# Kernel tuning notes

Measured on AMD Instinct MI355X. Metric: run time of the kernel, lower is better.

## Reference

```python
import jax, jax.numpy as jnp
import numpy as np

B, NB, C, FEAT = 2, 512, 80, 1024
FIRST_N = 128
NMS_FC = 128
POS_EMB = 64
GROUPS = 16
ATT_D = (1024, 1024, 128)
NUM_THRESH = 3
BBOX_W = (10.0, 10.0, 5.0, 5.0)
SCALE_CLAMP = float(np.log(1000.0 / 16.0))


def setup_inputs() -> dict:
    key = jax.random.key(0)
    ks = jax.random.split(key, 24)
    roi_feat = jax.random.normal(ks[0], (B * NB, FEAT), jnp.float32)
    scores = jax.random.normal(ks[1], (B * NB, C + 1), jnp.float32)
    proposal_deltas = jax.random.normal(ks[2], (B * NB, C * 4), jnp.float32) * 0.5
    xy = jax.random.uniform(ks[3], (B * NB, 2), jnp.float32) * 800.0
    wh = jax.random.uniform(ks[4], (B * NB, 2), jnp.float32) * 100.0 + 1.0
    proposal_boxes = jnp.concatenate([xy, xy + wh], axis=1)

    def lin(k, fin, fout, std=0.01):
        return jax.random.normal(k, (fin, fout), jnp.float32) * std

    return {
        'roi_feat': roi_feat,
        'scores': scores,
        'proposal_deltas': proposal_deltas,
        'proposal_boxes': proposal_boxes,
        'roi_w': lin(ks[5], FEAT, NMS_FC), 'roi_b': jnp.zeros((NMS_FC,), jnp.float32),
        'rank_w': lin(ks[6], FEAT, NMS_FC), 'rank_b': jnp.zeros((NMS_FC,), jnp.float32),
        'logit_w': lin(ks[7], NMS_FC, NUM_THRESH), 'logit_b': jnp.full((NUM_THRESH,), -3.0, jnp.float32),
        'pos_w': lin(ks[8], POS_EMB, GROUPS), 'pos_b': jnp.zeros((GROUPS,), jnp.float32),
        'q_w': lin(ks[9], NMS_FC, ATT_D[0]), 'q_b': jnp.zeros((ATT_D[0],), jnp.float32),
        'k_w': lin(ks[10], NMS_FC, ATT_D[1]), 'k_b': jnp.zeros((ATT_D[1],), jnp.float32),
        'out_w': jax.random.normal(ks[11], (GROUPS, NMS_FC, ATT_D[2] // GROUPS), jnp.float32) * 0.01,
        'out_b': jnp.zeros((ATT_D[2],), jnp.float32),
        'num_boxes': NB,
    }


def _rank_embedding():
    # sinusoidal rank embedding, dim FEAT
    fr = jnp.arange(FEAT // 2, dtype=jnp.float32)
    dim_mat = jnp.power(1000.0, (2.0 / FEAT) * fr)
    div = jnp.arange(FIRST_N, dtype=jnp.float32)[:, None] / dim_mat[None, :]
    return jnp.concatenate([jnp.sin(div), jnp.cos(div)], axis=1)  # (FIRST_N, FEAT)


def _pos_embed(boxes):
    # boxes: (FIRST_N, C, 4) -> (C, N, N, POS_EMB)
    b = jnp.transpose(boxes, (1, 0, 2))  # (C, N, 4)
    x1, y1, x2, y2 = b[..., 0], b[..., 1], b[..., 2], b[..., 3]
    w = x2 - x1 + 1.0
    h = y2 - y1 + 1.0
    cx = 0.5 * (x1 + x2)
    cy = 0.5 * (y1 + y2)
    dx = jnp.log(jnp.maximum(jnp.abs((cx[:, :, None] - cx[:, None, :]) / w[:, :, None]), 1e-3))
    dy = jnp.log(jnp.maximum(jnp.abs((cy[:, :, None] - cy[:, None, :]) / h[:, :, None]), 1e-3))
    dw = jnp.log(w[:, :, None] / w[:, None, :])
    dh = jnp.log(h[:, :, None] / h[:, None, :])
    pm = jnp.stack([dx, dy, dw, dh], axis=-1)  # (C, N, N, 4)
    fr = jnp.arange(POS_EMB // 8, dtype=jnp.float32)
    dim_mat = jnp.power(1000.0, (8.0 / POS_EMB) * fr)
    dv = (pm * 100.0)[..., None] / dim_mat  # (C, N, N, 4, POS_EMB//8)
    e = jnp.concatenate([jnp.sin(dv), jnp.cos(dv)], axis=-1)  # (C, N, N, 4, POS_EMB//4)
    return e.reshape(pm.shape[:3] + (POS_EMB,))


def reference(roi_feat, scores, proposal_deltas, proposal_boxes,
              roi_w, roi_b, rank_w, rank_b, logit_w, logit_b,
              pos_w, pos_b, q_w, q_b, k_w, k_b, out_w, out_b, num_boxes):
    deltas = jax.lax.stop_gradient(proposal_deltas)  # detached in original
    pboxes = jax.lax.stop_gradient(proposal_boxes)
    batch = deltas.shape[0] // num_boxes

    # ---- Box2BoxTransform.apply_deltas ----
    widths = pboxes[:, 2] - pboxes[:, 0]
    heights = pboxes[:, 3] - pboxes[:, 1]
    ctr_x = pboxes[:, 0] + 0.5 * widths
    ctr_y = pboxes[:, 1] + 0.5 * heights
    wx, wy, ww, wh = BBOX_W
    d = deltas.reshape(-1, C, 4)
    dx = d[..., 0] / wx
    dy = d[..., 1] / wy
    dw = jnp.minimum(d[..., 2] / ww, SCALE_CLAMP)
    dh = jnp.minimum(d[..., 3] / wh, SCALE_CLAMP)
    pcx = dx * widths[:, None] + ctr_x[:, None]
    pcy = dy * heights[:, None] + ctr_y[:, None]
    pw = jnp.exp(dw) * widths[:, None]
    ph = jnp.exp(dh) * heights[:, None]
    refined = jnp.stack([pcx - 0.5 * pw, pcy - 0.5 * ph, pcx + 0.5 * pw, pcy + 0.5 * ph], axis=-1)
    refined = refined.reshape(batch, num_boxes, C, 4)

    # ---- softmax + per-class descending sort, keep first_n ----
    sc = scores.reshape(batch, num_boxes, C + 1)
    probs = jax.nn.softmax(sc[..., :C], axis=1)
    rank_idxs = jnp.argsort(-probs, axis=1)[:, :FIRST_N, :]  # (B, FIRST_N, C)
    sorted_score = jnp.take_along_axis(probs, rank_idxs, axis=1)  # (B, FIRST_N, C)
    sorted_boxes = jax.vmap(lambda bx, i: jnp.take_along_axis(bx, i[..., None], axis=0))(refined, rank_idxs)  # (B, FIRST_N, C, 4)

    # ---- rank + roi embeddings ----
    rank_feat = _rank_embedding() @ rank_w + rank_b  # (FIRST_N, NMS_FC)
    roi_emb = (roi_feat @ roi_w + roi_b).reshape(batch, num_boxes, NMS_FC)
    sorted_roi = jax.vmap(lambda e, i: e[i])(roi_emb, rank_idxs)  # (B, FIRST_N, C, NMS_FC)
    emb_feat = sorted_roi + rank_feat[None, :, None, :]

    dq = ATT_D[0] // GROUPS
    dk = ATT_D[1] // GROUPS

    def attend(feat, boxes):
        # feat: (FIRST_N, C, NMS_FC), boxes: (FIRST_N, C, 4)
        pe = _pos_embed(boxes)  # (C, N, N, POS_EMB)
        aff_w = jax.nn.relu(pe @ pos_w + pos_b)  # (C, N, N, G)
        aff_w = jnp.transpose(aff_w, (0, 3, 1, 2))  # (C, G, N, N)
        f = jnp.transpose(feat, (1, 0, 2))  # (C, N, NMS_FC)
        q = (f @ q_w + q_b).reshape(C, FIRST_N, GROUPS, dq).transpose(0, 2, 1, 3)
        k = (f @ k_w + k_b).reshape(C, FIRST_N, GROUPS, dk).transpose(0, 2, 1, 3)
        aff = jnp.einsum('cgnd,cgmd->cgnm', q, k) / jnp.sqrt(jnp.float32(dk))
        sm = jax.nn.softmax(jnp.log(jnp.maximum(aff_w, 1e-6)) + aff, axis=-1)
        ov = jnp.einsum('cgnm,cmd->cgnd', sm, f)  # (C, G, N, NMS_FC)
        lin = jnp.einsum('cgnd,gde->cnge', ov, out_w).reshape(C, FIRST_N, ATT_D[2]) + out_b
        return jnp.transpose(lin, (1, 0, 2))  # (N, C, ATT_D[2])

    att = jax.vmap(attend)(emb_feat, sorted_boxes)
    all_feat = jax.nn.relu(emb_feat + att)
    logit = all_feat @ logit_w + logit_b  # (B, FIRST_N, C, NUM_THRESH)
    nms_multi_score = jax.nn.sigmoid(logit) * sorted_score[..., None]
    return nms_multi_score
```

## Files before the change

kernel.cpp:

```cpp
#include <hip/hip_runtime.h>
#include <math.h>

#define B_    2
#define NB_   512
#define C_    80
#define FEAT_ 1024
#define FN_   128
#define FC_   128
#define PE_   64
#define G_    16
#define DQ_   64
#define EO_   8
#define NT_   3
#define SCALE_CLAMP_ 4.135166556742356f

typedef __attribute__((ext_vector_type(8))) short bf16x8;
typedef __attribute__((ext_vector_type(4))) float f32x4;

#define O_ROIP    ((size_t)0)
#define O_RANKP   (O_ROIP + (size_t)4*B_*NB_*FC_)
#define O_RANKIDX (O_RANKP + (size_t)4*FN_*FC_)
#define O_SSCORE  (O_RANKIDX + (size_t)B_*FN_*C_)
#define O_SBOX    (O_SSCORE + (size_t)B_*FN_*C_)
#define O_EMB     (O_SBOX + (size_t)B_*FN_*C_*4)
#define O_ATT     (O_EMB + (size_t)B_*FN_*C_*FC_)
#define O_LW      (O_ATT + (size_t)B_*FN_*C_*FC_)
#define O_WT      (O_LW + (size_t)B_*C_*FN_*G_*FN_/2)
#define O_EMBB    (O_WT + (size_t)16*144*128/2)

__device__ __forceinline__ float bf2f(unsigned short u) {
    return __uint_as_float(((unsigned int)u) << 16);
}
__device__ __forceinline__ unsigned short f2bf(float f) {
    unsigned int x = __float_as_uint(f);
    unsigned int r = (x + 0x7fff + ((x >> 16) & 1)) >> 16;
    return (unsigned short)r;
}
__device__ __forceinline__ unsigned short f2h(float x) {
    _Float16 h = (_Float16)x;
    return __builtin_bit_cast(unsigned short, h);
}
__device__ __forceinline__ float h2f(unsigned short u) {
    _Float16 h = __builtin_bit_cast(_Float16, u);
    return (float)h;
}

#define ADDR128(row, gr)  ((row)*128 + ((((gr) ^ ((row)&7))) << 4))

__global__ __launch_bounds__(256) void k_embed(const float* __restrict__ roi_feat,
                                               const float* __restrict__ roi_w,
                                               const float* __restrict__ roi_b,
                                               const float* __restrict__ rank_w,
                                               const float* __restrict__ rank_b,
                                               const float* __restrict__ q_w,
                                               const float* __restrict__ k_w,
                                               const float* __restrict__ out_w,
                                               float* __restrict__ roiP,
                                               float* __restrict__ rankP,
                                               unsigned short* __restrict__ wtg)
{
    const int bid = blockIdx.x;
    const int t = threadIdx.x;
    if (bid >= 288) {
        const int g = bid - 288;
        for (int idx = t; idx < 144*16; idx += 256) {
            const int row = idx >> 4;
            const int kc  = (idx & 15) * 8;
            unsigned short u[8];
            if (row < 64) {
                #pragma unroll
                for (int j = 0; j < 8; ++j) u[j] = f2bf(q_w[(size_t)(kc + j)*1024 + g*DQ_ + row]);
            } else if (row < 128) {
                const int r = row - 64;
                #pragma unroll
                for (int j = 0; j < 8; ++j) u[j] = f2bf(k_w[(size_t)(kc + j)*1024 + g*DQ_ + r]);
            } else if (row < 136) {
                const int e = row - 128;
                #pragma unroll
                for (int j = 0; j < 8; ++j) u[j] = f2bf(out_w[(size_t)g*FC_*EO_ + (size_t)(kc + j)*EO_ + e]);
            } else {
                #pragma unroll
                for (int j = 0; j < 8; ++j) u[j] = 0;
            }
            *(uint4*)(wtg + (size_t)g*144*128 + row*128 + kc) =
                make_uint4((unsigned)u[0] | ((unsigned)u[1] << 16),
                           (unsigned)u[2] | ((unsigned)u[3] << 16),
                           (unsigned)u[4] | ((unsigned)u[5] << 16),
                           (unsigned)u[6] | ((unsigned)u[7] << 16));
        }
        return;
    }
    const int kq  = bid & 3;
    const int rt  = bid >> 2;
    const bool isRank = rt >= 64;
    const int row0 = (isRank ? rt - 64 : rt) * 16;
    const int w = t >> 6, lane = t & 63, lr = lane & 15, lh = lane >> 4;
    const int col0 = w * 32;
    const float* W = isRank ? rank_w : roi_w;
    const float* bias = isRank ? rank_b : roi_b;

    const int arow = row0 + lr;
    f32x4 acc0 = {0,0,0,0}, acc1 = {0,0,0,0};

    #pragma unroll 4
    for (int ks = 0; ks < 8; ++ks) {
        const int kb = kq*256 + ks*32 + lh*8;
        bf16x8 af;
        if (!isRank) {
            float4 a0 = *(const float4*)(roi_feat + (size_t)arow*FEAT_ + kb);
            float4 a1 = *(const float4*)(roi_feat + (size_t)arow*FEAT_ + kb + 4);
            af[0] = (short)f2bf(a0.x); af[1] = (short)f2bf(a0.y);
            af[2] = (short)f2bf(a0.z); af[3] = (short)f2bf(a0.w);
            af[4] = (short)f2bf(a1.x); af[5] = (short)f2bf(a1.y);
            af[6] = (short)f2bf(a1.z); af[7] = (short)f2bf(a1.w);
        } else {
            #pragma unroll
            for (int j = 0; j < 8; ++j) {
                int k = kb + j;
                int kk = k & 511;
                float inv = exp2f(-(float)kk * 0.0194644226f);
                float arg = (float)arow * inv;
                float v = (k < 512) ? __sinf(arg) : __cosf(arg);
                af[j] = (short)f2bf(v);
            }
        }
        bf16x8 bf0, bf1;
        #pragma unroll
        for (int j = 0; j < 8; ++j) {
            const float* wr = W + (size_t)(kb + j)*FC_ + col0 + lr;
            bf0[j] = (short)f2bf(wr[0]);
            bf1[j] = (short)f2bf(wr[16]);
        }
        acc0 = __builtin_amdgcn_mfma_f32_16x16x32_bf16(af, bf0, acc0, 0, 0, 0);
        acc1 = __builtin_amdgcn_mfma_f32_16x16x32_bf16(af, bf1, acc1, 0, 0, 0);
    }
    float* dst = isRank ? (rankP + (size_t)kq*FN_*FC_) : (roiP + (size_t)kq*(B_*NB_)*FC_);
    #pragma unroll
    for (int tile = 0; tile < 2; ++tile) {
        f32x4 a = tile ? acc1 : acc0;
        int col = col0 + tile*16 + lr;
        float bv = (kq == 0) ? bias[col] : 0.0f;
        #pragma unroll
        for (int reg = 0; reg < 4; ++reg) {
            int rr = row0 + lh*4 + reg;
            dst[(size_t)rr*FC_ + col] = a[reg] + bv;
        }
    }
}

__global__ __launch_bounds__(512) void k_topk(const float* __restrict__ scores,
                                              int* __restrict__ rank_idx,
                                              float* __restrict__ sorted_score)
{
    int b = blockIdx.x / C_, c = blockIdx.x % C_;
    __shared__ float p[NB_];
    __shared__ float red[NB_];
    int i = threadIdx.x;
    float s = scores[(size_t)(b*NB_ + i)*(C_+1) + c];
    red[i] = s; __syncthreads();
    for (int o = 256; o > 0; o >>= 1) { if (i < o) red[i] = fmaxf(red[i], red[i+o]); __syncthreads(); }
    float mx = red[0]; __syncthreads();
    float e = expf(s - mx);
    red[i] = e; __syncthreads();
    for (int o = 256; o > 0; o >>= 1) { if (i < o) red[i] += red[i+o]; __syncthreads(); }
    float sum = red[0]; __syncthreads();
    float pi = e / sum;
    p[i] = pi; __syncthreads();
    int rank = 0;
    for (int j4 = 0; j4 < NB_/4; ++j4) {
        float4 pj = *(const float4*)&p[j4*4];
        int j = j4*4;
        rank += (pj.x > pi) || (pj.x == pi && (j+0) < i);
        rank += (pj.y > pi) || (pj.y == pi && (j+1) < i);
        rank += (pj.z > pi) || (pj.z == pi && (j+2) < i);
        rank += (pj.w > pi) || (pj.w == pi && (j+3) < i);
    }
    if (rank < FN_) {
        rank_idx[(size_t)(b*FN_ + rank)*C_ + c] = i;
        sorted_score[(size_t)(b*FN_ + rank)*C_ + c] = pi;
    }
}

__global__ __launch_bounds__(256) void k_gather(const int* __restrict__ rank_idx,
                                                const float* __restrict__ roiP,
                                                const float* __restrict__ rankP,
                                                const float* __restrict__ pdeltas,
                                                const float* __restrict__ pboxes,
                                                float* __restrict__ emb_feat,
                                                unsigned short* __restrict__ embB,
                                                float* __restrict__ sorted_boxes)
{
    const int t = threadIdx.x;
    const int item = blockIdx.x*8 + (t >> 5);
    const int l = t & 31;
    const int c = item % C_;
    const int bn = item / C_;
    const int n = bn & (FN_-1);
    const int b = bn >> 7;
    const int idx = rank_idx[item];
    const int row = b*NB_ + idx;
    float4 sm = make_float4(0.f, 0.f, 0.f, 0.f);
    #pragma unroll
    for (int kq = 0; kq < 4; ++kq) {
        float4 e = *(const float4*)(roiP + (size_t)(kq*B_*NB_ + row)*FC_ + l*4);
        float4 r = *(const float4*)(rankP + (size_t)(kq*FN_ + n)*FC_ + l*4);
        sm.x += e.x + r.x; sm.y += e.y + r.y; sm.z += e.z + r.z; sm.w += e.w + r.w;
    }
    *(float4*)(emb_feat + (size_t)item*FC_ + l*4) = sm;
    *(uint2*)(embB + (size_t)item*FC_ + l*4) =
        make_uint2((unsigned)f2bf(sm.x) | ((unsigned)f2bf(sm.y) << 16),
                   (unsigned)f2bf(sm.z) | ((unsigned)f2bf(sm.w) << 16));
    if (l == 0) {
        float x1 = pboxes[row*4+0], y1 = pboxes[row*4+1], x2 = pboxes[row*4+2], y2 = pboxes[row*4+3];
        float w = x2 - x1, h = y2 - y1;
        float cx = x1 + 0.5f*w, cy = y1 + 0.5f*h;
        const float* dl = pdeltas + (size_t)row*(C_*4) + c*4;
        float dx = dl[0]/10.0f, dy = dl[1]/10.0f;
        float dw = fminf(dl[2]/5.0f, SCALE_CLAMP_);
        float dh = fminf(dl[3]/5.0f, SCALE_CLAMP_);
        float pcx = dx*w + cx, pcy = dy*h + cy;
        float pw = expf(dw)*w, ph = expf(dh)*h;
        float* ob = sorted_boxes + (size_t)item*4;
        ob[0] = pcx - 0.5f*pw; ob[1] = pcy - 0.5f*ph;
        ob[2] = pcx + 0.5f*pw; ob[3] = pcy + 0.5f*ph;
    }
}

__global__ __launch_bounds__(256) void k_pos2(const float* __restrict__ sorted_boxes,
                                              const float* __restrict__ pos_w,
                                              const float* __restrict__ pos_b,
                                              unsigned short* __restrict__ lw)
{
    const int n2   = blockIdx.x & 63;
    const int rest = blockIdx.x >> 6;
    const int cl   = rest % C_;
    const int b    = rest / C_;
    const int n0   = n2 * 2;
    const int t    = threadIdx.x;

    __shared__ float geomL[FN_][6];
    __shared__ unsigned short featL[256*PE_];
    __shared__ unsigned short poswL[G_*PE_];
    __shared__ float pbL[G_];
    __shared__ float sdimL[8];

    if (t < FN_) {
        const float* bx = sorted_boxes + (((size_t)(b*FN_ + t))*C_ + cl)*4;
        float x1 = bx[0], y1 = bx[1], x2 = bx[2], y2 = bx[3];
        float w = x2 - x1 + 1.0f;
        float h = y2 - y1 + 1.0f;
        geomL[t][0] = 0.5f*(x1+x2);
        geomL[t][1] = 0.5f*(y1+y2);
        geomL[t][2] = w;
        geomL[t][3] = h;
        geomL[t][4] = __logf(w);
        geomL[t][5] = __logf(h);
    } else {
        int id = t - 128;
        int g  = id >> 3;
        int gr = id & 7;
        unsigned short u[8];
        #pragma unroll
        for (int j = 0; j < 8; ++j) u[j] = f2bf(pos_w[(gr*8 + j)*G_ + g]);
        *(uint4*)((char*)poswL + ADDR128(g, gr)) =
            make_uint4((unsigned)u[0] | ((unsigned)u[1] << 16),
                       (unsigned)u[2] | ((unsigned)u[3] << 16),
                       (unsigned)u[4] | ((unsigned)u[5] << 16),
                       (unsigned)u[6] | ((unsigned)u[7] << 16));
    }
    if (t < G_) pbL[t] = pos_b[t];
    if (t >= 16 && t < 24) sdimL[t-16] = 1.0f / powf(1000.0f, 0.125f*(float)(t-16));
    __syncthreads();

    {
        const int nl = t >> 7;
        const int m  = t & 127;
        const int n  = n0 + nl;
        float pm[4];
        {
            float cxn = geomL[n][0], cyn = geomL[n][1];
            float rwn = 1.0f/geomL[n][2], rhn = 1.0f/geomL[n][3];
            pm[0] = __logf(fmaxf(fabsf((cxn - geomL[m][0]) * rwn), 1e-3f)) * 100.0f;
            pm[1] = __logf(fmaxf(fabsf((cyn - geomL[m][1]) * rhn), 1e-3f)) * 100.0f;
            pm[2] = (geomL[n][4] - geomL[m][4]) * 100.0f;
            pm[3] = (geomL[n][5] - geomL[m][5]) * 100.0f;
        }
        char* base = (char*)featL;
        #pragma unroll
        for (int f = 0; f < 4; ++f) {
            float s[8], c[8];
            #pragma unroll
            for (int r = 0; r < 8; ++r) {
                __sincosf(pm[f] * sdimL[r], &s[r], &c[r]);
            }
            unsigned short us[8], uc[8];
            #pragma unroll
            for (int r = 0; r < 8; ++r) { us[r] = f2bf(s[r]); uc[r] = f2bf(c[r]); }
            *(uint4*)(base + ADDR128(t, 2*f)) =
                make_uint4((unsigned)us[0] | ((unsigned)us[1] << 16),
                           (unsigned)us[2] | ((unsigned)us[3] << 16),
                           (unsigned)us[4] | ((unsigned)us[5] << 16),
                           (unsigned)us[6] | ((unsigned)us[7] << 16));
            *(uint4*)(base + ADDR128(t, 2*f + 1)) =
                make_uint4((unsigned)uc[0] | ((unsigned)uc[1] << 16),
                           (unsigned)uc[2] | ((unsigned)uc[3] << 16),
                           (unsigned)uc[4] | ((unsigned)uc[5] << 16),
                           (unsigned)uc[6] | ((unsigned)uc[7] << 16));
        }
    }
    __syncthreads();

    {
        const int wave = t >> 6, lane = t & 63;
        const int lr = lane & 15, lh = lane >> 4;
        const float pbg = pbL[lr];
        #pragma unroll
        for (int ti = 0; ti < 4; ++ti) {
            const int t16 = wave*4 + ti;
            f32x4 acc = {0,0,0,0};
            #pragma unroll
            for (int ks = 0; ks < 2; ++ks) {
                bf16x8 a  = *(const bf16x8*)((char*)featL + ADDR128(t16*16 + lr, ks*4 + lh));
                bf16x8 bb = *(const bf16x8*)((char*)poswL + ADDR128(lr, ks*4 + lh));
                acc = __builtin_amdgcn_mfma_f32_16x16x32_bf16(a, bb, acc, 0, 0, 0);
            }
            const int g = lr;
            #pragma unroll
            for (int reg = 0; reg < 4; ++reg) {
                int p = t16*16 + lh*4 + reg;
                int n = n0 + (p >> 7);
                int m = p & 127;
                float w = fmaxf(fmaxf(acc[reg] + pbg, 0.0f), 1e-6f);
                lw[(((size_t)(b*C_ + cl)*FN_ + n)*G_ + g)*FN_ + m] = f2h(__logf(w));
            }
        }
    }
}

#define FT_OFF   0
#define QL_OFF   34816
#define KL_OFF   51200
#define VT_OFF   67584
#define BIAS_OFF 71680
#define SMEM_SZ  72192

__global__ __launch_bounds__(1024, 8) void k_attn(const unsigned short* __restrict__ embB,
                                               const unsigned short* __restrict__ wt,
                                               const float* __restrict__ q_b,
                                               const float* __restrict__ k_b,
                                               const float* __restrict__ out_b,
                                               const unsigned short* __restrict__ lw,
                                               float* __restrict__ att)
{
    const int g    = blockIdx.x & 15;
    const int rest = blockIdx.x >> 4;
    const int cl   = rest % C_;
    const int b    = rest / C_;
    const int c    = cl;
    const int t  = threadIdx.x;
    const int wave = t >> 6;
    const int lane = t & 63;
    const int lr = lane & 15;
    const int lh = lane >> 4;

    __shared__ char smem[SMEM_SZ];
    float* biasL = (float*)(smem + BIAS_OFF);

    {
        const char* src = (const char*)embB + ((size_t)(b*FN_)*C_ + c)*FC_*2;
        #pragma unroll
        for (int s = 0; s < 2; ++s) {
            int fi = t + s*1024;
            int n  = fi >> 4;
            int o16 = (fi & 15) * 16;
            uint4 v = *(const uint4*)(src + (size_t)n*C_*FC_*2 + o16);
            *(uint4*)(smem + FT_OFF + n*272 + o16) = v;
        }
    }
    if (t >= 512 && t < 768) {
        int i = t - 512;
        *(uint2*)(smem + VT_OFF + 8*256 + i*8) = make_uint2(0u, 0u);
    }
    if (t >= 128 && t < 256) {
        int r = t - 128;
        biasL[r] = (r < 64) ? q_b[g*DQ_ + r] : k_b[g*DQ_ + (r-64)];
    }
    __syncthreads();

    {
        const int rb = (wave >> 2) * 32;
        const int nb = (wave & 3) * 32;
        const char* wtg = (const char*)wt + (size_t)g*144*256;
        f32x4 acc00 = {0,0,0,0}, acc01 = {0,0,0,0}, acc10 = {0,0,0,0}, acc11 = {0,0,0,0};
        f32x4 accV  = {0,0,0,0};
        #pragma unroll
        for (int ks = 0; ks < 4; ++ks) {
            const int fo = ks*64 + lh*16;
            bf16x8 a0 = *(const bf16x8*)(wtg + (rb + lr)*256 + fo);
            bf16x8 a1 = *(const bf16x8*)(wtg + (rb + 16 + lr)*256 + fo);
            bf16x8 b0 = *(const bf16x8*)(smem + FT_OFF + (nb + lr)*272 + fo);
            bf16x8 b1 = *(const bf16x8*)(smem + FT_OFF + (nb + 16 + lr)*272 + fo);
            acc00 = __builtin_amdgcn_mfma_f32_16x16x32_bf16(a0, b0, acc00, 0, 0, 0);
            acc01 = __builtin_amdgcn_mfma_f32_16x16x32_bf16(a0, b1, acc01, 0, 0, 0);
            acc10 = __builtin_amdgcn_mfma_f32_16x16x32_bf16(a1, b0, acc10, 0, 0, 0);
            acc11 = __builtin_amdgcn_mfma_f32_16x16x32_bf16(a1, b1, acc11, 0, 0, 0);
            if (wave < 8) {
                bf16x8 av = *(const bf16x8*)(wtg + (128 + lr)*256 + fo);
                bf16x8 bv = *(const bf16x8*)(smem + FT_OFF + (wave*16 + lr)*272 + fo);
                accV = __builtin_amdgcn_mfma_f32_16x16x32_bf16(av, bv, accV, 0, 0, 0);
            }
        }
        #pragma unroll
        for (int ti = 0; ti < 2; ++ti) {
            #pragma unroll
            for (int tj = 0; tj < 2; ++tj) {
                f32x4 a = (ti == 0) ? (tj == 0 ? acc00 : acc01) : (tj == 0 ? acc10 : acc11);
                int r0 = rb + ti*16 + lh*4;
                int n  = nb + tj*16 + lr;
                float v0 = a[0] + biasL[r0+0];
                float v1 = a[1] + biasL[r0+1];
                float v2 = a[2] + biasL[r0+2];
                float v3 = a[3] + biasL[r0+3];
                int dq0 = r0 & 63;
                int off = (r0 < 64 ? QL_OFF : KL_OFF);
                char* dst = smem + off + ADDR128(n, dq0 >> 3) + ((dq0 >> 2) & 1)*8;
                *(uint2*)dst = make_uint2((unsigned)f2bf(v0) | ((unsigned)f2bf(v1) << 16),
                                          (unsigned)f2bf(v2) | ((unsigned)f2bf(v3) << 16));
            }
        }
        if (wave < 8 && lh < 2) {
            int m = wave*16 + lr;
            #pragma unroll
            for (int reg = 0; reg < 4; ++reg) {
                int e = lh*4 + reg;
                char* dst = smem + VT_OFF + (e)*256 + ((((m >> 3) ^ e)) << 4) + (m & 7)*2;
                *(unsigned short*)dst = f2bf(accV[reg]);
            }
        }
    }
    __syncthreads();

    uint4 gl0, gl1;
    {
        const int row_p = t >> 3;
        const int lp_p  = t & 7;
        const unsigned short* lwrow = lw + ((((size_t)(b*C_ + cl))*FN_ + row_p)*G_ + g)*FN_ + lp_p*16;
        gl0 = *(const uint4*)(lwrow);
        gl1 = *(const uint4*)(lwrow + 8);
    }
    {
        const int nb = (wave >> 2) * 32;
        const int mb = (wave & 3) * 32;
        f32x4 acc00 = {0,0,0,0}, acc01 = {0,0,0,0}, acc10 = {0,0,0,0}, acc11 = {0,0,0,0};
        #pragma unroll
        for (int ks = 0; ks < 2; ++ks) {
            int soff = ((ks*4 + lh) ^ (lr & 7)) << 4;
            bf16x8 a0 = *(const bf16x8*)(smem + QL_OFF + (nb + lr)*128 + soff);
            bf16x8 a1 = *(const bf16x8*)(smem + QL_OFF + (nb + 16 + lr)*128 + soff);
            bf16x8 b0 = *(const bf16x8*)(smem + KL_OFF + (mb + lr)*128 + soff);
            bf16x8 b1 = *(const bf16x8*)(smem + KL_OFF + (mb + 16 + lr)*128 + soff);
            acc00 = __builtin_amdgcn_mfma_f32_16x16x32_bf16(a0, b0, acc00, 0, 0, 0);
            acc01 = __builtin_amdgcn_mfma_f32_16x16x32_bf16(a0, b1, acc01, 0, 0, 0);
            acc10 = __builtin_amdgcn_mfma_f32_16x16x32_bf16(a1, b0, acc10, 0, 0, 0);
            acc11 = __builtin_amdgcn_mfma_f32_16x16x32_bf16(a1, b1, acc11, 0, 0, 0);
        }
        #pragma unroll
        for (int ti = 0; ti < 2; ++ti) {
            #pragma unroll
            for (int tj = 0; tj < 2; ++tj) {
                f32x4 a = (ti == 0) ? (tj == 0 ? acc00 : acc01) : (tj == 0 ? acc10 : acc11);
                int n0 = nb + ti*16 + lh*4;
                int m  = mb + tj*16 + lr;
                #pragma unroll
                for (int reg = 0; reg < 4; ++reg)
                    *(unsigned short*)(smem + FT_OFF + (n0 + reg)*272 + 2*m) = f2h(a[reg]);
            }
        }
    }
    __syncthreads();

    {
        const int row = t >> 3;
        const int lp  = t & 7;
        char* abase = smem + FT_OFF + row*272 + lp*32;
        uint4 af0 = *(const uint4*)abase;
        uint4 af1 = *(const uint4*)(abase + 16);
        const unsigned short* ah0 = (const unsigned short*)&af0;
        const unsigned short* ah1 = (const unsigned short*)&af1;
        const unsigned short* lp0 = (const unsigned short*)&gl0;
        const unsigned short* lp1 = (const unsigned short*)&gl1;
        float v[16];
        float mx = -INFINITY;
        #pragma unroll
        for (int j = 0; j < 8; ++j) {
            float val = h2f(ah0[j])*0.125f + h2f(lp0[j]);
            v[j] = val; mx = fmaxf(mx, val);
        }
        #pragma unroll
        for (int j = 0; j < 8; ++j) {
            float val = h2f(ah1[j])*0.125f + h2f(lp1[j]);
            v[8+j] = val; mx = fmaxf(mx, val);
        }
        #pragma unroll
        for (int s = 1; s < 8; s <<= 1) mx = fmaxf(mx, __shfl_xor(mx, s, 8));
        float sum = 0.f;
        #pragma unroll
        for (int j = 0; j < 16; ++j) { v[j] = __expf(v[j] - mx); sum += v[j]; }
        #pragma unroll
        for (int s = 1; s < 8; s <<= 1) sum += __shfl_xor(sum, s, 8);
        float rs = 1.0f / sum;
        unsigned short u[16];
        #pragma unroll
        for (int j = 0; j < 16; ++j) u[j] = f2bf(v[j] * rs);
        *(uint4*)abase = make_uint4((unsigned)u[0] | ((unsigned)u[1] << 16),
                                    (unsigned)u[2] | ((unsigned)u[3] << 16),
                                    (unsigned)u[4] | ((unsigned)u[5] << 16),
                                    (unsigned)u[6] | ((unsigned)u[7] << 16));
        *(uint4*)(abase + 16) = make_uint4((unsigned)u[8]  | ((unsigned)u[9]  << 16),
                                           (unsigned)u[10] | ((unsigned)u[11] << 16),
                                           (unsigned)u[12] | ((unsigned)u[13] << 16),
                                           (unsigned)u[14] | ((unsigned)u[15] << 16));
    }
    __syncthreads();

    if (wave < 8) {
        const int tb = wave * 16;
        f32x4 acc = {0,0,0,0};
        #pragma unroll
        for (int ks = 0; ks < 4; ++ks) {
            const int fo = ks*64 + lh*16;
            int soff = ((ks*4 + lh) ^ lr) << 4;
            bf16x8 a = *(const bf16x8*)(smem + FT_OFF + (tb + lr)*272 + fo);
            bf16x8 bv = *(const bf16x8*)(smem + VT_OFF + lr*256 + soff);
            acc = __builtin_amdgcn_mfma_f32_16x16x32_bf16(a, bv, acc, 0, 0, 0);
        }
        if (lr < 8) {
            float ob = out_b[g*EO_ + lr];
            #pragma unroll
            for (int reg = 0; reg < 4; ++reg) {
                int n = tb + lh*4 + reg;
                att[((size_t)(b*FN_ + n)*C_ + c)*FC_ + g*EO_ + lr] = acc[reg] + ob;
            }
        }
    }
}

__global__ __launch_bounds__(256) void k_final(const float* __restrict__ emb_feat,
                                               const float* __restrict__ att,
                                               const float* __restrict__ logit_w,
                                               const float* __restrict__ logit_b,
                                               const float* __restrict__ sorted_score,
                                               float* __restrict__ out)
{
    __shared__ float lwL[FC_*NT_ + NT_];
    const int t = threadIdx.x;
    for (int i = t; i < FC_*NT_ + NT_; i += 256)
        lwL[i] = (i < FC_*NT_) ? logit_w[i] : logit_b[i - FC_*NT_];
    __syncthreads();
    const int item = blockIdx.x*8 + (t >> 5);
    const int l = t & 31;
    const int d0 = l*4;
    float4 ev = *(const float4*)(emb_feat + (size_t)item*FC_ + d0);
    float4 av = *(const float4*)(att + (size_t)item*FC_ + d0);
    float a0 = fmaxf(ev.x + av.x, 0.f);
    float a1 = fmaxf(ev.y + av.y, 0.f);
    float a2 = fmaxf(ev.z + av.z, 0.f);
    float a3 = fmaxf(ev.w + av.w, 0.f);
    float s0 = a0*lwL[(d0+0)*NT_+0] + a1*lwL[(d0+1)*NT_+0] + a2*lwL[(d0+2)*NT_+0] + a3*lwL[(d0+3)*NT_+0];
    float s1 = a0*lwL[(d0+0)*NT_+1] + a1*lwL[(d0+1)*NT_+1] + a2*lwL[(d0+2)*NT_+1] + a3*lwL[(d0+3)*NT_+1];
    float s2 = a0*lwL[(d0+0)*NT_+2] + a1*lwL[(d0+1)*NT_+2] + a2*lwL[(d0+2)*NT_+2] + a3*lwL[(d0+3)*NT_+2];
    #pragma unroll
    for (int s = 1; s < 32; s <<= 1) {
        s0 += __shfl_xor(s0, s, 32);
        s1 += __shfl_xor(s1, s, 32);
        s2 += __shfl_xor(s2, s, 32);
    }
    if (l < NT_) {
        float lg = (l == 0) ? s0 : (l == 1) ? s1 : s2;
        lg += lwL[FC_*NT_ + l];
        float sg = 1.f / (1.f + expf(-lg));
        out[(size_t)item*NT_ + l] = sg * sorted_score[item];
    }
}

extern "C" void kernel_launch(void* const* d_in, const int* in_sizes, int n_in,
                              void* d_out, int out_size, void* d_ws, size_t ws_size,
                              hipStream_t stream) {
    (void)in_sizes; (void)n_in; (void)out_size; (void)ws_size;
    const float* roi_feat = (const float*)d_in[0];
    const float* scores   = (const float*)d_in[1];
    const float* pdeltas  = (const float*)d_in[2];
    const float* pboxes   = (const float*)d_in[3];
    const float* roi_w    = (const float*)d_in[4];
    const float* roi_b    = (const float*)d_in[5];
    const float* rank_w   = (const float*)d_in[6];
    const float* rank_b   = (const float*)d_in[7];
    const float* logit_w  = (const float*)d_in[8];
    const float* logit_b  = (const float*)d_in[9];
    const float* pos_w    = (const float*)d_in[10];
    const float* pos_b    = (const float*)d_in[11];
    const float* q_w      = (const float*)d_in[12];
    const float* q_b      = (const float*)d_in[13];
    const float* k_w      = (const float*)d_in[14];
    const float* k_b      = (const float*)d_in[15];
    const float* out_w    = (const float*)d_in[16];
    const float* out_b    = (const float*)d_in[17];
    float* ws = (float*)d_ws;

    float* roiP         = ws + O_ROIP;
    float* rankP        = ws + O_RANKP;
    int*   rank_idx     = (int*)(ws + O_RANKIDX);
    float* sorted_score = ws + O_SSCORE;
    float* sorted_boxes = ws + O_SBOX;
    float* emb_feat     = ws + O_EMB;
    float* att          = ws + O_ATT;
    unsigned short* lwb = (unsigned short*)(ws + O_LW);
    unsigned short* wtb = (unsigned short*)(ws + O_WT);
    unsigned short* embB = (unsigned short*)(ws + O_EMBB);

    k_embed<<<dim3(304), dim3(256), 0, stream>>>(roi_feat, roi_w, roi_b, rank_w, rank_b,
                                                 q_w, k_w, out_w, roiP, rankP, wtb);
    k_topk<<<dim3(B_*C_), dim3(512), 0, stream>>>(scores, rank_idx, sorted_score);
    k_gather<<<dim3(B_*FN_*C_/8), dim3(256), 0, stream>>>(rank_idx, roiP, rankP,
                                                          pdeltas, pboxes, emb_feat, embB, sorted_boxes);
    k_pos2<<<dim3(B_*C_*64), dim3(256), 0, stream>>>(sorted_boxes, pos_w, pos_b, lwb);
    k_attn<<<dim3(B_*C_*G_), dim3(1024), 0, stream>>>(embB, wtb, q_b, k_b, out_b, lwb, att);
    k_final<<<dim3(B_*FN_*C_/8), dim3(256), 0, stream>>>(emb_feat, att, logit_w, logit_b,
                                                         sorted_score, d_out ? (float*)d_out : nullptr);
}
```

Before: 183.6 us.

## Fuse top-k ranking with embedding gather into one kernel

Merges the per-class softmax/rank kernel with the gather kernel, so the selected indices stay in shared memory and are never round-tripped through global memory. This also drops one kernel launch. The max and sum reductions now use wavefront shuffles instead of shared-memory tree reductions. The cost is that the gather work, previously spread over 2560 blocks, now runs in only 160 blocks of 512 threads, which reduces parallelism for the memory-bound gather.

Result: no change. 182.6 us, median of 2 (-0.6%).

```diff
diff --git a/kernel.cpp b/kernel.cpp
--- a/kernel.cpp
+++ b/kernel.cpp
@@ -19,8 +19,7 @@
 
 #define O_ROIP    ((size_t)0)
 #define O_RANKP   (O_ROIP + (size_t)4*B_*NB_*FC_)
-#define O_RANKIDX (O_RANKP + (size_t)4*FN_*FC_)
-#define O_SSCORE  (O_RANKIDX + (size_t)B_*FN_*C_)
+#define O_SSCORE  (O_RANKP + (size_t)4*FN_*FC_)
 #define O_SBOX    (O_SSCORE + (size_t)B_*FN_*C_)
 #define O_EMB     (O_SBOX + (size_t)B_*FN_*C_*4)
 #define O_ATT     (O_EMB + (size_t)B_*FN_*C_*FC_)
@@ -148,69 +147,88 @@
     }
 }
 
-__global__ __launch_bounds__(512) void k_topk(const float* __restrict__ scores,
-                                              int* __restrict__ rank_idx,
-                                              float* __restrict__ sorted_score)
+__global__ __launch_bounds__(512) void k_topkgather(const float* __restrict__ scores,
+                                                    const float* __restrict__ roiP,
+                                                    const float* __restrict__ rankP,
+                                                    const float* __restrict__ pdeltas,
+                                                    const float* __restrict__ pboxes,
+                                                    float* __restrict__ sorted_score,
+                                                    float* __restrict__ emb_feat,
+                                                    unsigned short* __restrict__ embB,
+                                                    float* __restrict__ sorted_boxes)
 {
-    int b = blockIdx.x / C_, c = blockIdx.x % C_;
+    const int b = blockIdx.x / C_, c = blockIdx.x % C_;
     __shared__ float p[NB_];
-    __shared__ float red[NB_];
-    int i = threadIdx.x;
-    float s = scores[(size_t)(b*NB_ + i)*(C_+1) + c];
-    red[i] = s; __syncthreads();
-    for (int o = 256; o > 0; o >>= 1) { if (i < o) red[i] = fmaxf(red[i], red[i+o]); __syncthreads(); }
-    float mx = red[0]; __syncthreads();
+    __shared__ float wred[8];
+    __shared__ int   sidxL[FN_];
+    const int t = threadIdx.x;
+    const int lane = t & 63, wv = t >> 6;
+
+    float s = scores[(size_t)(b*NB_ + t)*(C_+1) + c];
+    float mx = s;
+    #pragma unroll
+    for (int o = 1; o < 64; o <<= 1) mx = fmaxf(mx, __shfl_xor(mx, o, 64));
+    if (lane == 0) wred[wv] = mx;
+    __syncthreads();
+    mx = wred[0];
+    #pragma unroll
+    for (int j = 1; j < 8; ++j) mx = fmaxf(mx, wred[j]);
     float e = expf(s - mx);
-    red[i] = e; __syncthreads();
-    for (int o = 256; o > 0; o >>= 1) { if (i < o) red[i] += red[i+o]; __syncthreads(); }
-    float sum = red[0]; __syncthreads();
+    float ws_ = e;
+    #pragma unroll
+    for (int o = 1; o < 64; o <<= 1) ws_ += __shfl_xor(ws_, o, 64);
+    __syncthreads();
+    if (lane == 0) wred[wv] = ws_;
+    __syncthreads();
+    float sum = 0.f;
+    #pragma unroll
+    for (int j = 0; j < 8; ++j) sum += wred[j];
     float pi = e / sum;
-    p[i] = pi; __syncthreads();
+    p[t] = pi;
+    __syncthreads();
+
     int rank = 0;
     for (int j4 = 0; j4 < NB_/4; ++j4) {
         float4 pj = *(const float4*)&p[j4*4];
         int j = j4*4;
-        rank += (pj.x > pi) || (pj.x == pi && (j+0) < i);
-        rank += (pj.y > pi) || (pj.y == pi && (j+1) < i);
-        rank += (pj.z > pi) || (pj.z == pi && (j+2) < i);
-        rank += (pj.w > pi) || (pj.w == pi && (j+3) < i);
+        rank += (pj.x > pi) || (pj.x == pi && (j+0) < t);
+        rank += (pj.y > pi) || (pj.y == pi && (j+1) < t);
+        rank += (pj.z > pi) || (pj.z == pi && (j+2) < t);
+        rank += (pj.w > pi) || (pj.w == pi && (j+3) < t);
     }
     if (rank < FN_) {
-        rank_idx[(size_t)(b*FN_ + rank)*C_ + c] = i;
+        sidxL[rank] = t;
         sorted_score[(size_t)(b*FN_ + rank)*C_ + c] = pi;
     }
-}
-
-__global__ __launch_bounds__(256) void k_gather(const int* __restrict__ rank_idx,
-                                                const float* __restrict__ roiP,
-                                                const float* __restrict__ rankP,
-                                                const float* __restrict__ pdeltas,
-                                                const float* __restrict__ pboxes,
-                                                float* __restrict__ emb_feat,
-                                                unsigned short* __restrict__ embB,
-                                                float* __restrict__ sorted_boxes)
-{
-    const int t = threadIdx.x;
-    const int item = blockIdx.x*8 + (t >> 5);
-    const int l = t & 31;
-    const int c = item % C_;
-    const int bn = item / C_;
-    const int n = bn & (FN_-1);
-    const int b = bn >> 7;
-    const int idx = rank_idx[item];
-    const int row = b*NB_ + idx;
-    float4 sm = make_float4(0.f, 0.f, 0.f, 0.f);
-    #pragma unroll
-    for (int kq = 0; kq < 4; ++kq) {
-        float4 e = *(const float4*)(roiP + (size_t)(kq*B_*NB_ + row)*FC_ + l*4);
-        float4 r = *(const float4*)(rankP + (size_t)(kq*FN_ + n)*FC_ + l*4);
-        sm.x += e.x + r.x; sm.y += e.y + r.y; sm.z += e.z + r.z; sm.w += e.w + r.w;
-    }
-    *(float4*)(emb_feat + (size_t)item*FC_ + l*4) = sm;
-    *(uint2*)(embB + (size_t)item*FC_ + l*4) =
-        make_uint2((unsigned)f2bf(sm.x) | ((unsigned)f2bf(sm.y) << 16),
-                   (unsigned)f2bf(sm.z) | ((unsigned)f2bf(sm.w) << 16));
-    if (l == 0) {
+    __syncthreads();
+
+    {
+        const int slot = t >> 5;
+        const int l = t & 31;
+        #pragma unroll
+        for (int iter = 0; iter < 8; ++iter) {
+            const int r = slot + 16*iter;
+            const int idx = sidxL[r];
+            const int row = b*NB_ + idx;
+            float4 sm = make_float4(0.f, 0.f, 0.f, 0.f);
+            #pragma unroll
+            for (int kq = 0; kq < 4; ++kq) {
+                float4 ev = *(const float4*)(roiP + (size_t)(kq*B_*NB_ + row)*FC_ + l*4);
+                float4 rv = *(const float4*)(rankP + (size_t)(kq*FN_ + r)*FC_ + l*4);
+                sm.x += ev.x + rv.x; sm.y += ev.y + rv.y;
+                sm.z += ev.z + rv.z; sm.w += ev.w + rv.w;
+            }
+            const size_t itemoff = ((size_t)(b*FN_ + r)*C_ + c)*FC_;
+            *(float4*)(emb_feat + itemoff + l*4) = sm;
+            *(uint2*)(embB + itemoff + l*4) =
+                make_uint2((unsigned)f2bf(sm.x) | ((unsigned)f2bf(sm.y) << 16),
+                           (unsigned)f2bf(sm.z) | ((unsigned)f2bf(sm.w) << 16));
+        }
+    }
+    if (t < FN_) {
+        const int r = t;
+        const int idx = sidxL[r];
+        const int row = b*NB_ + idx;
         float x1 = pboxes[row*4+0], y1 = pboxes[row*4+1], x2 = pboxes[row*4+2], y2 = pboxes[row*4+3];
         float w = x2 - x1, h = y2 - y1;
         float cx = x1 + 0.5f*w, cy = y1 + 0.5f*h;
@@ -220,6 +238,7 @@
         float dh = fminf(dl[3]/5.0f, SCALE_CLAMP_);
         float pcx = dx*w + cx, pcy = dy*h + cy;
         float pw = expf(dw)*w, ph = expf(dh)*h;
+        const int item = (b*FN_ + r)*C_ + c;
         float* ob = sorted_boxes + (size_t)item*4;
         ob[0] = pcx - 0.5f*pw; ob[1] = pcy - 0.5f*ph;
         ob[2] = pcx + 0.5f*pw; ob[3] = pcy + 0.5f*ph;
@@ -609,7 +628,6 @@
 
     float* roiP         = ws + O_ROIP;
     float* rankP        = ws + O_RANKP;
-    int*   rank_idx     = (int*)(ws + O_RANKIDX);
     float* sorted_score = ws + O_SSCORE;
     float* sorted_boxes = ws + O_SBOX;
     float* emb_feat     = ws + O_EMB;
@@ -620,9 +638,8 @@
 
     k_embed<<<dim3(304), dim3(256), 0, stream>>>(roi_feat, roi_w, roi_b, rank_w, rank_b,
                                                  q_w, k_w, out_w, roiP, rankP, wtb);
-    k_topk<<<dim3(B_*C_), dim3(512), 0, stream>>>(scores, rank_idx, sorted_score);
-    k_gather<<<dim3(B_*FN_*C_/8), dim3(256), 0, stream>>>(rank_idx, roiP, rankP,
-                                                          pdeltas, pboxes, emb_feat, embB, sorted_boxes);
+    k_topkgather<<<dim3(B_*C_), dim3(512), 0, stream>>>(scores, roiP, rankP, pdeltas, pboxes,
+                                                        sorted_score, emb_feat, embB, sorted_boxes);
     k_pos2<<<dim3(B_*C_*64), dim3(256), 0, stream>>>(sorted_boxes, pos_w, pos_b, lwb);
     k_attn<<<dim3(B_*C_*G_), dim3(1024), 0, stream>>>(embB, wtb, q_b, k_b, out_b, lwb, att);
     k_final<<<dim3(B_*FN_*C_/8), dim3(256), 0, stream>>>(emb_feat, att, logit_w, logit_b,
```
